# Kernel optimization log

Hardware: AMD Instinct MI355X
Metric: run time of the kernel (lower is better)

The kernel has to match this reference:

```python
import jax, jax.numpy as jnp
import numpy as np

MAX_RADIUS = 0.9
TEMP = 0.1

def _to_poincare(x, W, b):
    # Linear + Tanh, then rescale into Poincare ball of radius 0.9
    h = jnp.tanh(x @ W.T + b)
    norm = jnp.clip(jnp.linalg.norm(h, axis=-1, keepdims=True), 1e-8, None)
    scale = jnp.where(norm > MAX_RADIUS, MAX_RADIUS / norm, jnp.ones_like(norm))
    return h * scale

def setup_inputs() -> dict:
    key = jax.random.key(0)
    kq, kw, kb, km, ko = jax.random.split(key, 5)
    B, N, D = 2048, 100000, 128
    return {
        "query": jax.random.normal(kq, (B, D), dtype=jnp.float32),
        "W": jax.random.normal(kw, (D, D), dtype=jnp.float32) * (1.0 / np.sqrt(D)),
        "b": jax.random.normal(kb, (D,), dtype=jnp.float32) * 0.01,
        "mem_emb": jax.random.normal(km, (N, D), dtype=jnp.float32),
        "mem_out": jax.random.normal(ko, (N, D), dtype=jnp.float32),
        "k": 16,
    }

def reference(query, W, b, mem_emb, mem_out, k):
    q = _to_poincare(query, W, b)          # [B, D]
    m = _to_poincare(mem_emb, W, b)        # [N, D]
    # Euclidean cdist via the GEMM form: ||q||^2 + ||m||^2 - 2 q.m
    q2 = jnp.sum(q * q, axis=-1, keepdims=True)           # [B, 1]
    m2 = jnp.sum(m * m, axis=-1)                          # [N]
    d2 = q2 + m2[None, :] - 2.0 * (q @ m.T)               # [B, N]
    dists = jnp.sqrt(jnp.maximum(d2, 1e-12))
    # k smallest distances
    neg_top, top_idx = jax.lax.top_k(-dists, k)           # [B, k]
    top_dists = -neg_top
    weights = jax.nn.softmax(-top_dists / TEMP, axis=-1)  # [B, k]
    outcomes = mem_out[top_idx]                           # [B, k, D]
    return weights, outcomes
```

## Files before the change

kernel.cpp:

```cpp
#include <hip/hip_runtime.h>
#include <hip/hip_bf16.h>
#include <math.h>

#define DIM 128
#define QB 128
#define MB 64
#define NSPLIT 32
#define KSEL 16
#define KOWN 4
#define RESCORE 32
#define IDXMASK 0x1FFFu
#define KEYMASK 0xFFFFE000u
#define M2MAX 3200

using bf16x8 = __attribute__((ext_vector_type(8))) short;
using f32x4  = __attribute__((ext_vector_type(4))) float;

__device__ inline unsigned short f2bf(float f) {
  __hip_bfloat16 h = __float2bfloat16(f);
  return __builtin_bit_cast(unsigned short, h);
}
__device__ inline unsigned uminu(unsigned a, unsigned b) {
  return __builtin_elementwise_min(a, b);
}
__device__ inline unsigned umaxu(unsigned a, unsigned b) {
  return __builtin_elementwise_max(a, b);
}
__device__ inline unsigned long long umin64(unsigned long long a,
                                            unsigned long long b) {
  return __builtin_elementwise_min(a, b);
}

__device__ inline f32x4 mfma16(bf16x8 a, bf16x8 b, f32x4 c) {
  return __builtin_amdgcn_mfma_f32_16x16x32_bf16(a, b, c, 0, 0, 0);
}

__device__ inline void gload_lds16(const void* g, void* l) {
  __builtin_amdgcn_global_load_lds(
      (const __attribute__((address_space(1))) void*)g,
      (__attribute__((address_space(3))) void*)l, 16, 0, 0);
}

__device__ inline void ins4(unsigned (&ks)[KOWN], unsigned c) {
  #pragma unroll
  for (int i = 0; i < KOWN; ++i) {
    const unsigned lo = uminu(c, ks[i]);
    c = umaxu(c, ks[i]);
    ks[i] = lo;
  }
}

__global__ __launch_bounds__(512) void poincare2_k(
    const float* __restrict__ Xm, int Rm,
    const float* __restrict__ Xq, int Rq,
    const float* __restrict__ W, const float* __restrict__ bias,
    float* __restrict__ Pm, float* __restrict__ Pm2,
    float* __restrict__ Pm2s, int npadm,
    unsigned short* __restrict__ Pmbf,
    float* __restrict__ Pq, float* __restrict__ Pq2, int nbm)
{
  __shared__ float Wl[DIM * DIM];
  __shared__ float nrm[128 * 17];
  __shared__ float norm2l[128];

  const int t  = threadIdx.x;
  const int cg = t & 15;
  const int rg = t >> 4;

  const bool ismem = (int)blockIdx.x < nbm;
  const float* X = ismem ? Xm : Xq;
  const int    R = ismem ? Rm : Rq;
  float*       P  = ismem ? Pm  : Pq;
  float*       P2 = ismem ? Pm2 : Pq2;
  unsigned short* Pbf = ismem ? Pmbf : nullptr;
  const int rbase = (ismem ? blockIdx.x : (blockIdx.x - nbm)) * 128;

  for (int i = t; i < DIM * 32; i += 512) {
    const int j = i >> 5, c = i & 31;
    const float4 v = *(const float4*)&W[j * DIM + c * 4];
    *(float4*)&Wl[j * DIM + ((c ^ ((j >> 3) & 7)) << 2)] = v;
  }
  float bj[8];
  #pragma unroll
  for (int u = 0; u < 8; ++u) bj[u] = bias[cg * 8 + u];

  const float* xr[4];
  #pragma unroll
  for (int v = 0; v < 4; ++v) {
    int row = rbase + rg + 32 * v;
    if (row > R - 1) row = R - 1;
    xr[v] = X + (size_t)row * DIM;
  }
  __syncthreads();

  float acc[4][8];
  #pragma unroll
  for (int v = 0; v < 4; ++v)
    #pragma unroll
    for (int u = 0; u < 8; ++u) acc[v][u] = bj[u];

  #pragma unroll 2
  for (int k4 = 0; k4 < 32; ++k4) {
    float4 xv[4], wv[8];
    #pragma unroll
    for (int v = 0; v < 4; ++v) xv[v] = *(const float4*)&xr[v][k4 * 4];
    #pragma unroll
    for (int u = 0; u < 8; ++u) {
      const int j = cg * 8 + u;
      wv[u] = *(const float4*)&Wl[j * DIM + ((k4 ^ ((j >> 3) & 7)) << 2)];
    }
    #pragma unroll
    for (int v = 0; v < 4; ++v)
      #pragma unroll
      for (int u = 0; u < 8; ++u) {
        acc[v][u] = fmaf(xv[v].x, wv[u].x, acc[v][u]);
        acc[v][u] = fmaf(xv[v].y, wv[u].y, acc[v][u]);
        acc[v][u] = fmaf(xv[v].z, wv[u].z, acc[v][u]);
        acc[v][u] = fmaf(xv[v].w, wv[u].w, acc[v][u]);
      }
  }

  #pragma unroll
  for (int v = 0; v < 4; ++v) {
    float pn = 0.f;
    #pragma unroll
    for (int u = 0; u < 8; ++u) {
      const float th = tanhf(acc[v][u]);
      acc[v][u] = th;
      pn = fmaf(th, th, pn);
    }
    nrm[(rg + 32 * v) * 17 + cg] = pn;
  }
  __syncthreads();
  if (t < 128) {
    float s = 0.f;
    #pragma unroll
    for (int c2 = 0; c2 < 16; ++c2) s += nrm[t * 17 + c2];
    norm2l[t] = s;
    const int row = rbase + t;
    if (row < R) {
      const float nm = sqrtf(s);
      const float sc = (nm > 0.9f) ? (0.9f / nm) : 1.0f;
      const float p2v = s * sc * sc;
      P2[row] = p2v;
      if (ismem) Pm2s[row] = fmaf(0.5f, p2v, 1.0f);
    } else if (ismem && row < npadm) {
      Pm2s[row] = __int_as_float(0x7f800000);
    }
  }
  __syncthreads();

  #pragma unroll
  for (int v = 0; v < 4; ++v) {
    const int r = rg + 32 * v;
    const int row = rbase + r;
    if (row < R) {
      const float n2 = norm2l[r];
      const float nm = sqrtf(n2);
      const float sc = (nm > 0.9f) ? (0.9f / nm) : 1.0f;
      float o[8];
      #pragma unroll
      for (int u = 0; u < 8; ++u) o[u] = acc[v][u] * sc;
      *(float4*)&P[(size_t)row * DIM + cg * 8]     = make_float4(o[0], o[1], o[2], o[3]);
      *(float4*)&P[(size_t)row * DIM + cg * 8 + 4] = make_float4(o[4], o[5], o[6], o[7]);
      if (Pbf) {
        uint4 pb;
        pb.x = (unsigned)f2bf(o[0]) | ((unsigned)f2bf(o[1]) << 16);
        pb.y = (unsigned)f2bf(o[2]) | ((unsigned)f2bf(o[3]) << 16);
        pb.z = (unsigned)f2bf(o[4]) | ((unsigned)f2bf(o[5]) << 16);
        pb.w = (unsigned)f2bf(o[6]) | ((unsigned)f2bf(o[7]) << 16);
        *(uint4*)&Pmbf[(size_t)row * DIM + ((cg ^ (row & 15)) << 3)] = pb;
      }
    }
  }
}

template<bool USEBF>
__global__ __launch_bounds__(512, 2) void score_topk_k(
    const float* __restrict__ Pq,
    const float* __restrict__ Pm, const float* __restrict__ Pm2s,
    const unsigned short* __restrict__ Pmbf,
    int N, int splitlen, unsigned* __restrict__ splitTop)
{
  __shared__ __align__(16) unsigned short Ml[3][MB * DIM];
  __shared__ float m2all[M2MAX];

  const int t = threadIdx.x;
  const int lane = t & 63;
  const int w = t >> 6, wr = w >> 1, wc = w & 1;
  const int split = blockIdx.x;
  const int qbase = blockIdx.y * QB;
  const int mlo = split * splitlen;
  const int mhi = min(mlo + splitlen, N);
  const int ntiles = (mhi - mlo + MB - 1) / MB;

  bf16x8 qf[2][4];
  #pragma unroll
  for (int s = 0; s < 2; ++s) {
    const int qrow = qbase + wr * 32 + s * 16 + (lane & 15);
    #pragma unroll
    for (int ks = 0; ks < 4; ++ks) {
      const float* src = &Pq[(size_t)qrow * DIM + ks * 32 + (lane >> 4) * 8];
      float4 lo = *(const float4*)src;
      float4 hi = *(const float4*)(src + 4);
      bf16x8 v;
      v[0] = (short)f2bf(-lo.x); v[1] = (short)f2bf(-lo.y);
      v[2] = (short)f2bf(-lo.z); v[3] = (short)f2bf(-lo.w);
      v[4] = (short)f2bf(-hi.x); v[5] = (short)f2bf(-hi.y);
      v[6] = (short)f2bf(-hi.z); v[7] = (short)f2bf(-hi.w);
      qf[s][ks] = v;
    }
  }

  for (int i = t; i < splitlen; i += 512) m2all[i] = Pm2s[mlo + i];

  const size_t soff0 = (size_t)(w * 8 + (lane >> 4)) * DIM + ((lane & 15) << 3);
  const size_t soff1 = soff0 + 4 * DIM;

  auto stageU = [&](int tilei, int buf) {
    const unsigned short* b = Pmbf + (size_t)(mlo + tilei * MB) * DIM;
    gload_lds16(b + soff0, &Ml[buf][(w * 8) * DIM]);
    gload_lds16(b + soff1, &Ml[buf][(w * 8 + 4) * DIM]);
  };
  uint4 sv0, sv1;
  auto stageF_load = [&](int tilei) {
    const int fr = t >> 3, fe = t & 7;
    const float* src = Pm + (size_t)(mlo + tilei * MB + fr) * DIM + fe * 16;
    float4 a0 = *(const float4*)(src + 0);
    float4 a1 = *(const float4*)(src + 4);
    float4 a2 = *(const float4*)(src + 8);
    float4 a3 = *(const float4*)(src + 12);
    sv0.x = (unsigned)f2bf(a0.x) | ((unsigned)f2bf(a0.y) << 16);
    sv0.y = (unsigned)f2bf(a0.z) | ((unsigned)f2bf(a0.w) << 16);
    sv0.z = (unsigned)f2bf(a1.x) | ((unsigned)f2bf(a1.y) << 16);
    sv0.w = (unsigned)f2bf(a1.z) | ((unsigned)f2bf(a1.w) << 16);
    sv1.x = (unsigned)f2bf(a2.x) | ((unsigned)f2bf(a2.y) << 16);
    sv1.y = (unsigned)f2bf(a2.z) | ((unsigned)f2bf(a2.w) << 16);
    sv1.z = (unsigned)f2bf(a3.x) | ((unsigned)f2bf(a3.y) << 16);
    sv1.w = (unsigned)f2bf(a3.z) | ((unsigned)f2bf(a3.w) << 16);
  };
  auto stageF_write = [&](int buf) {
    const int fr = t >> 3, fe = t & 7;
    char* base = (char*)&Ml[buf][0] + fr * 256;
    *(uint4*)(base + (((2 * fe)     ^ (fr & 15)) << 4)) = sv0;
    *(uint4*)(base + (((2 * fe + 1) ^ (fr & 15)) << 4)) = sv1;
  };

  unsigned keys[2][4][KOWN];
  #pragma unroll
  for (int s = 0; s < 2; ++s)
    #pragma unroll
    for (int r = 0; r < 4; ++r)
      #pragma unroll
      for (int i = 0; i < KOWN; ++i) keys[s][r][i] = 0xFFFFFFFFu;

  const int mcol = wc * 32 + (lane & 15);
  const int rowA = mcol, rowB = mcol + 16;

  auto compute = [&](int tile, const unsigned short* cur) {
    const float ca = m2all[tile * MB + mcol];
    const float cb = m2all[tile * MB + mcol + 16];
    f32x4 a00 = (f32x4){ca, ca, ca, ca};
    f32x4 a01 = (f32x4){cb, cb, cb, cb};
    f32x4 a10 = (f32x4){ca, ca, ca, ca};
    f32x4 a11 = (f32x4){cb, cb, cb, cb};
    __builtin_amdgcn_s_setprio(1);
    #pragma unroll
    for (int ks = 0; ks < 4; ++ks) {
      const int kb = ks * 64 + (lane >> 4) * 16;
      bf16x8 bfrA = *(const bf16x8*)((const char*)cur + rowA * 256 +
                                     (kb ^ ((rowA & 15) << 4)));
      bf16x8 bfrB = *(const bf16x8*)((const char*)cur + rowB * 256 +
                                     (kb ^ ((rowB & 15) << 4)));
      a00 = mfma16(qf[0][ks], bfrA, a00);
      a01 = mfma16(qf[0][ks], bfrB, a01);
      a10 = mfma16(qf[1][ks], bfrA, a10);
      a11 = mfma16(qf[1][ks], bfrB, a11);
    }
    __builtin_amdgcn_s_setprio(0);
    const unsigned idx0 = (unsigned)(tile * MB + mcol);
    #pragma unroll
    for (int r = 0; r < 4; ++r) {
      ins4(keys[0][r], (__float_as_uint(a00[r]) & KEYMASK) | idx0);
      ins4(keys[0][r], (__float_as_uint(a01[r]) & KEYMASK) | (idx0 + 16));
      ins4(keys[1][r], (__float_as_uint(a10[r]) & KEYMASK) | idx0);
      ins4(keys[1][r], (__float_as_uint(a11[r]) & KEYMASK) | (idx0 + 16));
    }
  };

  if constexpr (USEBF) {
    __syncthreads();
    stageU(0, 0);
    if (ntiles > 1) stageU(1, 1);
    int cur = 0;
    for (int i = 0; i < ntiles; ++i) {
      if (i < ntiles - 1) asm volatile("s_waitcnt vmcnt(2)" ::: "memory");
      else                asm volatile("s_waitcnt vmcnt(0)" ::: "memory");
      __builtin_amdgcn_s_barrier();
      __builtin_amdgcn_sched_barrier(0);
      int nb = cur + 2; if (nb >= 3) nb -= 3;
      if (i + 2 < ntiles) stageU(i + 2, nb);
      compute(i, &Ml[cur][0]);
      cur = (cur + 1 == 3) ? 0 : cur + 1;
    }
  } else {
    stageF_load(0);
    stageF_write(0);
    __syncthreads();
    for (int i = 0; i < ntiles; ++i) {
      const int cur = i & 1;
      const bool more = (i + 1 < ntiles);
      if (more) stageF_load(i + 1);
      compute(i, &Ml[cur][0]);
      __syncthreads();
      if (more) stageF_write(cur ^ 1);
      __syncthreads();
    }
  }

  unsigned* mb = (unsigned*)&Ml[0][0];
  __syncthreads();
  #pragma unroll
  for (int s = 0; s < 2; ++s)
    #pragma unroll
    for (int r = 0; r < 4; ++r) {
      unsigned k0 = keys[s][r][0], k1 = keys[s][r][1];
      unsigned k2 = keys[s][r][2], k3 = keys[s][r][3];
      unsigned out = 0xFFFFFFFFu;
      for (int round = 0; round < 8; ++round) {
        unsigned g = k0;
        g = uminu(g, __shfl_xor(g, 1, 16));
        g = uminu(g, __shfl_xor(g, 2, 16));
        g = uminu(g, __shfl_xor(g, 4, 16));
        g = uminu(g, __shfl_xor(g, 8, 16));
        const bool mine = (k0 == g);
        k0 = mine ? k1 : k0;
        k1 = mine ? k2 : k1;
        k2 = mine ? k3 : k2;
        k3 = mine ? 0xFFFFFFFFu : k3;
        if ((lane & 15) == round) out = g;
      }
      const int lq = wr * 32 + s * 16 + (lane >> 4) * 4 + r;
      if ((lane & 15) < 8) mb[lq * 16 + wc * 8 + (lane & 15)] = out;
    }
  __syncthreads();
  if (wc == 0 && lane < 32) {
    const int lq = wr * 32 + lane;
    unsigned s8[8];
    #pragma unroll
    for (int i = 0; i < 8; ++i) s8[i] = 0xFFFFFFFFu;
    const unsigned* src = mb + lq * 16;
    #pragma unroll
    for (int i = 0; i < 16; ++i) {
      unsigned c = src[i];
      #pragma unroll
      for (int j = 0; j < 8; ++j) {
        const unsigned lo = uminu(c, s8[j]);
        c = umaxu(c, s8[j]);
        s8[j] = lo;
      }
    }
    unsigned* dst = &splitTop[((size_t)(qbase + lq) * NSPLIT + split) * 8];
    *(uint4*)dst       = make_uint4(s8[0], s8[1], s8[2], s8[3]);
    *((uint4*)dst + 1) = make_uint4(s8[4], s8[5], s8[6], s8[7]);
  }
}

__global__ __launch_bounds__(256) void finalize_k(
    const unsigned* __restrict__ splitTop,
    const float* __restrict__ Pq, const float* __restrict__ Pq2,
    const float* __restrict__ Pm, const float* __restrict__ Pm2,
    const float* __restrict__ memOut, int N, int splitlen,
    float* __restrict__ outW, float* __restrict__ outO)
{
  const int wv   = threadIdx.x >> 6;
  const int lane = threadIdx.x & 63;
  const int q = blockIdx.x * 4 + wv;

  __shared__ unsigned      sKey[4][RESCORE];
  __shared__ unsigned char sSrc[4][RESCORE];
  __shared__ unsigned long long sKeyx[4][RESCORE];
  __shared__ unsigned long long sSel[4][KSEL];
  __shared__ float sEl[4][KSEL];

  {
    unsigned a[8];
    if (lane < NSPLIT) {
      const unsigned* gp = splitTop + (size_t)q * (NSPLIT * 8) + lane * 8;
      uint4 lo = *(const uint4*)gp;
      uint4 hi = *(const uint4*)(gp + 4);
      a[0] = lo.x; a[1] = lo.y; a[2] = lo.z; a[3] = lo.w;
      a[4] = hi.x; a[5] = hi.y; a[6] = hi.z; a[7] = hi.w;
    } else {
      #pragma unroll
      for (int i = 0; i < 8; ++i) a[i] = 0xFFFFFFFFu;
    }
    for (int r = 0; r < RESCORE; ++r) {
      unsigned g = a[0];
      g = uminu(g, __shfl_xor(g, 1));
      g = uminu(g, __shfl_xor(g, 2));
      g = uminu(g, __shfl_xor(g, 4));
      g = uminu(g, __shfl_xor(g, 8));
      g = uminu(g, __shfl_xor(g, 16));
      g = uminu(g, __shfl_xor(g, 32));
      unsigned long long mask = __ballot(a[0] == g);
      const int fl = __ffsll((unsigned long long)mask) - 1;
      if (lane == fl) {
        #pragma unroll
        for (int i = 0; i < 7; ++i) a[i] = a[i + 1];
        a[7] = 0xFFFFFFFFu;
      }
      if (lane == 0) { sKey[wv][r] = g; sSrc[wv][r] = (unsigned char)fl; }
    }
  }

  #pragma unroll
  for (int p = 0; p < 4; ++p) {
    const int g8 = p * 8 + (lane >> 3), e = lane & 7;
    const int gidx = (int)sSrc[wv][g8] * splitlen + (int)(sKey[wv][g8] & IDXMASK);
    const float4* qr = (const float4*)&Pq[(size_t)q * DIM];
    const float4* mr = (const float4*)&Pm[(size_t)gidx * DIM];
    float s = 0.f;
    #pragma unroll
    for (int u = 0; u < 4; ++u) {
      float4 a = qr[e * 4 + u], b = mr[e * 4 + u];
      s = fmaf(a.x, b.x, s); s = fmaf(a.y, b.y, s);
      s = fmaf(a.z, b.z, s); s = fmaf(a.w, b.w, s);
    }
    s += __shfl_xor(s, 1, 8);
    s += __shfl_xor(s, 2, 8);
    s += __shfl_xor(s, 4, 8);
    if (e == 0) {
      float d2 = (Pq2[q] + Pm2[gidx]) - 2.0f * s;
      float dist = sqrtf(fmaxf(d2, 1e-12f));
      sKeyx[wv][g8] =
          (((unsigned long long)__float_as_uint(dist)) << 32) | (unsigned)gidx;
    }
  }

  {
    unsigned long long kk = (lane < RESCORE) ? sKeyx[wv][lane] : ~0ull;
    for (int r = 0; r < KSEL; ++r) {
      unsigned long long g = kk;
      g = umin64(g, __shfl_xor(g, 1));
      g = umin64(g, __shfl_xor(g, 2));
      g = umin64(g, __shfl_xor(g, 4));
      g = umin64(g, __shfl_xor(g, 8));
      g = umin64(g, __shfl_xor(g, 16));
      g = umin64(g, __shfl_xor(g, 32));
      if (kk == g) kk = ~0ull;
      if (lane == 0) sSel[wv][r] = g;
    }
  }

  if (lane < KSEL) {
    const float d  = __uint_as_float((unsigned)(sSel[wv][lane] >> 32));
    const float d0 = __uint_as_float((unsigned)(sSel[wv][0] >> 32));
    sEl[wv][lane] = expf((d0 - d) * 10.0f);
  }
  if (lane < KSEL) {
    float sum = 0.f;
    #pragma unroll
    for (int i = 0; i < KSEL; ++i) sum += sEl[wv][i];
    outW[(size_t)q * KSEL + lane] = sEl[wv][lane] / sum;
  }

  #pragma unroll
  for (int i = 0; i < 8; ++i) {
    const int f4 = lane + i * 64;
    const int r = f4 >> 5, c4 = f4 & 31;
    const int idx = (int)(sSel[wv][r] & 0xffffffffu);
    *(float4*)&outO[((size_t)q * KSEL + r) * DIM + c4 * 4] =
        *(const float4*)&memOut[(size_t)idx * DIM + c4 * 4];
  }
}

extern "C" void kernel_launch(void* const* d_in, const int* in_sizes, int n_in,
                              void* d_out, int out_size, void* d_ws, size_t ws_size,
                              hipStream_t stream)
{
  const float* query   = (const float*)d_in[0];
  const float* W       = (const float*)d_in[1];
  const float* bias    = (const float*)d_in[2];
  const float* mem_emb = (const float*)d_in[3];
  const float* mem_out = (const float*)d_in[4];
  const int B = in_sizes[0] / DIM;
  const int N = in_sizes[3] / DIM;

  const int splitlen = ((N + NSPLIT * MB - 1) / (NSPLIT * MB)) * MB;
  const int N_pad2 = NSPLIT * splitlen;

  float* ws  = (float*)d_ws;
  float* Pm  = ws;
  float* Pm2 = Pm + (size_t)N * DIM;
  float* Pm2s = Pm2 + N;
  float* Pq  = Pm2s + N_pad2;
  float* Pq2 = Pq + (size_t)B * DIM;
  unsigned* splitTop = (unsigned*)(Pq2 + B);
  unsigned short* Pmbf = (unsigned short*)(splitTop + (size_t)B * NSPLIT * 8);
  const size_t need_bf = (size_t)((char*)(Pmbf + (size_t)N_pad2 * DIM) - (char*)d_ws);
  const bool usebf = ws_size >= need_bf;

  float* outW = (float*)d_out;
  float* outO = outW + (size_t)B * KSEL;

  const int nbm = (N_pad2 + 127) / 128;
  const int nbq = (B + 127) / 128;
  poincare2_k<<<dim3(nbm + nbq), dim3(512), 0, stream>>>(
      mem_emb, N, query, B, W, bias, Pm, Pm2, Pm2s, N_pad2,
      usebf ? Pmbf : nullptr, Pq, Pq2, nbm);

  dim3 grid2(NSPLIT, B / QB);
  if (usebf)
    score_topk_k<true><<<grid2, dim3(512), 0, stream>>>(Pq, Pm, Pm2s, Pmbf, N,
                                                        splitlen, splitTop);
  else
    score_topk_k<false><<<grid2, dim3(512), 0, stream>>>(Pq, Pm, Pm2s, nullptr, N,
                                                         splitlen, splitTop);

  finalize_k<<<dim3(B / 4), dim3(256), 0, stream>>>(splitTop, Pq, Pq2, Pm, Pm2,
                                                    mem_out, N, splitlen,
                                                    outW, outO);
}
```

Baseline: 214.0 us.

## Stage input rows in LDS and read W via wave-uniform scalar loads in projection

The Poincare projection kernel now stages the 128 input rows in shared memory instead of W. Each wave owns 16 output columns and reads W through wave-uniform addresses that can become scalar loads, while each lane computes two rows. The tanh results are written back into the same LDS buffer so the output stage can reuse the old row/column mapping. This removes per-lane redundant global X reads and the LDS W traffic, but it adds an extra sync and LDS round trip and makes W reads go through global or scalar cache.

```diff
diff --git a/kernel.cpp b/kernel.cpp
--- a/kernel.cpp
+++ b/kernel.cpp
@@ -59,13 +59,14 @@
     unsigned short* __restrict__ Pmbf,
     float* __restrict__ Pq, float* __restrict__ Pq2, int nbm)
 {
-  __shared__ float Wl[DIM * DIM];
-  __shared__ float nrm[128 * 17];
+  __shared__ float Xl[128 * DIM];
+  __shared__ float nrm[128 * 8];
   __shared__ float norm2l[128];
 
   const int t  = threadIdx.x;
-  const int cg = t & 15;
-  const int rg = t >> 4;
+  const int l  = t & 63;
+  const int wv_ = t >> 6;
+  const int jw = __builtin_amdgcn_readfirstlane(wv_ * 16);
 
   const bool ismem = (int)blockIdx.x < nbm;
   const float* X = ismem ? Xm : Xq;
@@ -75,67 +76,68 @@
   unsigned short* Pbf = ismem ? Pmbf : nullptr;
   const int rbase = (ismem ? blockIdx.x : (blockIdx.x - nbm)) * 128;
 
-  for (int i = t; i < DIM * 32; i += 512) {
-    const int j = i >> 5, c = i & 31;
-    const float4 v = *(const float4*)&W[j * DIM + c * 4];
-    *(float4*)&Wl[j * DIM + ((c ^ ((j >> 3) & 7)) << 2)] = v;
-  }
-  float bj[8];
-  #pragma unroll
-  for (int u = 0; u < 8; ++u) bj[u] = bias[cg * 8 + u];
-
-  const float* xr[4];
-  #pragma unroll
-  for (int v = 0; v < 4; ++v) {
-    int row = rbase + rg + 32 * v;
-    if (row > R - 1) row = R - 1;
-    xr[v] = X + (size_t)row * DIM;
+  for (int i = t; i < 128 * 32; i += 512) {
+    const int r = i >> 5, c = i & 31;
+    int row = rbase + r; if (row > R - 1) row = R - 1;
+    const float4 v = *(const float4*)&X[(size_t)row * DIM + c * 4];
+    *(float4*)&Xl[r * DIM + ((c ^ ((r >> 1) & 7)) << 2)] = v;
+  }
+
+  float acc0[16], acc1[16];
+  #pragma unroll
+  for (int u = 0; u < 16; ++u) {
+    const float b = bias[jw + u];
+    acc0[u] = b; acc1[u] = b;
   }
   __syncthreads();
 
-  float acc[4][8];
-  #pragma unroll
-  for (int v = 0; v < 4; ++v)
-    #pragma unroll
-    for (int u = 0; u < 8; ++u) acc[v][u] = bj[u];
-
+  const float* Wb = W + jw * DIM;
+  const int x0 = (2 * l) * DIM;
+  const int x1 = x0 + DIM;
   #pragma unroll 2
   for (int k4 = 0; k4 < 32; ++k4) {
-    float4 xv[4], wv[8];
-    #pragma unroll
-    for (int v = 0; v < 4; ++v) xv[v] = *(const float4*)&xr[v][k4 * 4];
-    #pragma unroll
-    for (int u = 0; u < 8; ++u) {
-      const int j = cg * 8 + u;
-      wv[u] = *(const float4*)&Wl[j * DIM + ((k4 ^ ((j >> 3) & 7)) << 2)];
-    }
-    #pragma unroll
-    for (int v = 0; v < 4; ++v)
-      #pragma unroll
-      for (int u = 0; u < 8; ++u) {
-        acc[v][u] = fmaf(xv[v].x, wv[u].x, acc[v][u]);
-        acc[v][u] = fmaf(xv[v].y, wv[u].y, acc[v][u]);
-        acc[v][u] = fmaf(xv[v].z, wv[u].z, acc[v][u]);
-        acc[v][u] = fmaf(xv[v].w, wv[u].w, acc[v][u]);
-      }
-  }
-
-  #pragma unroll
-  for (int v = 0; v < 4; ++v) {
-    float pn = 0.f;
-    #pragma unroll
-    for (int u = 0; u < 8; ++u) {
-      const float th = tanhf(acc[v][u]);
-      acc[v][u] = th;
-      pn = fmaf(th, th, pn);
-    }
-    nrm[(rg + 32 * v) * 17 + cg] = pn;
+    const int ch = (k4 ^ (l & 7)) << 2;
+    const float4 xv0 = *(const float4*)&Xl[x0 + ch];
+    const float4 xv1 = *(const float4*)&Xl[x1 + ch];
+    #pragma unroll
+    for (int u = 0; u < 16; ++u) {
+      const float4 wvv = *(const float4*)(Wb + u * DIM + k4 * 4);
+      acc0[u] = fmaf(xv0.x, wvv.x, acc0[u]);
+      acc0[u] = fmaf(xv0.y, wvv.y, acc0[u]);
+      acc0[u] = fmaf(xv0.z, wvv.z, acc0[u]);
+      acc0[u] = fmaf(xv0.w, wvv.w, acc0[u]);
+      acc1[u] = fmaf(xv1.x, wvv.x, acc1[u]);
+      acc1[u] = fmaf(xv1.y, wvv.y, acc1[u]);
+      acc1[u] = fmaf(xv1.z, wvv.z, acc1[u]);
+      acc1[u] = fmaf(xv1.w, wvv.w, acc1[u]);
+    }
+  }
+
+  float pn0 = 0.f, pn1 = 0.f;
+  #pragma unroll
+  for (int u = 0; u < 16; ++u) {
+    acc0[u] = tanhf(acc0[u]); pn0 = fmaf(acc0[u], acc0[u], pn0);
+    acc1[u] = tanhf(acc1[u]); pn1 = fmaf(acc1[u], acc1[u], pn1);
+  }
+  __syncthreads();
+  {
+    const int cb = jw >> 2;
+    #pragma unroll
+    for (int u4 = 0; u4 < 4; ++u4) {
+      const int pos = ((cb + u4) ^ (l & 7)) << 2;
+      *(float4*)&Xl[x0 + pos] = make_float4(acc0[u4*4], acc0[u4*4+1],
+                                            acc0[u4*4+2], acc0[u4*4+3]);
+      *(float4*)&Xl[x1 + pos] = make_float4(acc1[u4*4], acc1[u4*4+1],
+                                            acc1[u4*4+2], acc1[u4*4+3]);
+    }
+    nrm[(2 * l) * 8 + wv_]     = pn0;
+    nrm[(2 * l + 1) * 8 + wv_] = pn1;
   }
   __syncthreads();
   if (t < 128) {
     float s = 0.f;
     #pragma unroll
-    for (int c2 = 0; c2 < 16; ++c2) s += nrm[t * 17 + c2];
+    for (int j = 0; j < 8; ++j) s += nrm[t * 8 + j];
     norm2l[t] = s;
     const int row = rbase + t;
     if (row < R) {
@@ -150,6 +152,7 @@
   }
   __syncthreads();
 
+  const int cg = t & 15, rg = t >> 4;
   #pragma unroll
   for (int v = 0; v < 4; ++v) {
     const int r = rg + 32 * v;
@@ -158,9 +161,11 @@
       const float n2 = norm2l[r];
       const float nm = sqrtf(n2);
       const float sc = (nm > 0.9f) ? (0.9f / nm) : 1.0f;
-      float o[8];
-      #pragma unroll
-      for (int u = 0; u < 8; ++u) o[u] = acc[v][u] * sc;
+      const int sw = (r >> 1) & 7;
+      const float4 h0 = *(const float4*)&Xl[r * DIM + (((2*cg)   ^ sw) << 2)];
+      const float4 h1 = *(const float4*)&Xl[r * DIM + (((2*cg+1) ^ sw) << 2)];
+      float o[8] = {h0.x*sc, h0.y*sc, h0.z*sc, h0.w*sc,
+                    h1.x*sc, h1.y*sc, h1.z*sc, h1.w*sc};
       *(float4*)&P[(size_t)row * DIM + cg * 8]     = make_float4(o[0], o[1], o[2], o[3]);
       *(float4*)&P[(size_t)row * DIM + cg * 8 + 4] = make_float4(o[4], o[5], o[6], o[7]);
       if (Pbf) {
```

Measured after the change: 221.9 us. 3.7% more time.
